# Performance work log

Hardware: AMD Instinct MI355X
Metric: run time of the kernel (lower is better)

The kernel has to match this reference:

```python
import jax, jax.numpy as jnp
import numpy as np
import itertools


def _interpn_linear(vol, loc):
    """Trilinear interpolation of vol [D,H,W,C] at absolute coords loc [D,H,W,3].
    Matches neurite's interpn: clip coords to volume, floor/ceil corners, 8-corner
    weighted sum (nearest-extrapolation at borders)."""
    D, H, W, C = vol.shape
    max_idx = jnp.asarray([D - 1, H - 1, W - 1], dtype=loc.dtype)
    loc = jnp.clip(loc, 0.0, max_idx)
    loc0 = jnp.floor(loc)
    loc1 = jnp.minimum(loc0 + 1.0, max_idx)
    d1 = loc1 - loc                     # weight of corner 0 (floor)
    d0 = 1.0 - d1                       # weight of corner 1 (ceil)
    w = jnp.stack([d1, d0], axis=0)     # [2, D,H,W,3]
    idx = jnp.stack([loc0, loc1], axis=0).astype(jnp.int32)  # [2, D,H,W,3]
    vol_flat = vol.reshape(-1, C)
    out = jnp.zeros(loc.shape[:-1] + (C,), vol.dtype)
    for c in itertools.product((0, 1), repeat=3):  # fixed 8-corner loop
        flat = (idx[c[0], ..., 0] * H + idx[c[1], ..., 1]) * W + idx[c[2], ..., 2]
        wt = w[c[0], ..., 0] * w[c[1], ..., 1] * w[c[2], ..., 2]
        out = out + wt[..., None] * vol_flat[flat]
    return out


def _warp(vol, shift):
    """Sample dense field vol [D,H,W,3] at grid + shift (voxelmorph transform())."""
    D, H, W, _ = shift.shape
    grid = jnp.stack(
        jnp.meshgrid(jnp.arange(D), jnp.arange(H), jnp.arange(W), indexing='ij'),
        axis=-1,
    ).astype(shift.dtype)
    return _interpn_linear(vol, grid + shift)


def _compose(transforms):
    """voxelmorph utils.compose for dense transforms: T(x) = C(B(A(x))).
    curr = curr + warp(nxt, curr), folding right-to-left."""
    curr = transforms[-1]
    for nxt in reversed(transforms[:-1]):
        curr = curr + jax.vmap(_warp)(nxt, curr)
    return curr


def setup_inputs() -> dict:
    key = jax.random.key(0)
    k1, k2, k3 = jax.random.split(key, 3)
    shape = (2, 128, 160, 192, 3)  # [B, D, H, W, ndims] dense displacement fields
    scale = 3.0  # ~3-voxel displacements, realistic registration magnitude
    return {
        't1': scale * jax.random.normal(k1, shape, dtype=jnp.float32),
        't2': scale * jax.random.normal(k2, shape, dtype=jnp.float32),
        't3': scale * jax.random.normal(k3, shape, dtype=jnp.float32),
    }


def reference(t1, t2, t3):
    # Transforms listed in application order A, B, C -> T(x) = C(B(A(x)))
    return _compose([t1, t2, t3])
```

## Files before the change

### kernel.cpp

```cpp
#include <hip/hip_runtime.h>
#include <hip/hip_fp16.h>


#define BB 2
#define DD 128
#define HH 160
#define WW 192

#define WT_TILES 3
#define HT_TILES 80
#define DT_TILES 32
#define NBLOCKS (WT_TILES * HT_TILES * DT_TILES * BB)
#define PER_XCD (NBLOCKS / 8)

static __device__ __forceinline__ float3 cvt_h4(uint2 q) {
    float2 fa = __half22float2(*(const __half2*)&q.x);
    float  fz = __half2float(*(const __half*)&q.y);
    return make_float3(fa.x, fa.y, fz);
}

__global__ __launch_bounds__(256) void conv_f16_kernel(
    const float4* __restrict__ src, uint2* __restrict__ dst)
{
    __shared__ float4 lds4[768];
    const float* lds = (const float*)lds4;

    long base = (long)blockIdx.x * 1024;
    const float4* s4 = src + (long)blockIdx.x * 768;
    int tid = threadIdx.x;

#pragma unroll
    for (int j = 0; j < 3; ++j)
        lds4[tid + 256 * j] = s4[tid + 256 * j];
    __syncthreads();

#pragma unroll
    for (int j = 0; j < 4; ++j) {
        int v = tid + 256 * j;
        float x = lds[3 * v], y = lds[3 * v + 1], z = lds[3 * v + 2];
        uint2 q;
        q.x = (unsigned)__half_as_ushort(__float2half_rn(x)) |
              ((unsigned)__half_as_ushort(__float2half_rn(y)) << 16);
        q.y = (unsigned)__half_as_ushort(__float2half_rn(z));
        dst[base + v] = q;
    }
}

static __device__ __forceinline__ void interp_one(
    const uint2* __restrict__ baseq, int d, int h, int w,
    float sx, float sy, float sz, float& ox, float& oy, float& oz)
{
    float lx = fminf(fmaxf((float)d + sx, 0.f), (float)(DD - 1));
    float ly = fminf(fmaxf((float)h + sy, 0.f), (float)(HH - 1));
    float lz = fminf(fmaxf((float)w + sz, 0.f), (float)(WW - 1));

    float fx = floorf(lx), fy = floorf(ly), fz = floorf(lz);
    int x0 = (int)fx, y0 = (int)fy, z0 = (int)fz;
    int x1 = min(x0 + 1, DD - 1);
    int y1 = min(y0 + 1, HH - 1);

    int  z0m = min(z0, WW - 2);
    bool zhi = (z0 == WW - 1);

    float wx0 = (float)x1 - lx;
    float wy0 = (float)y1 - ly;
    float wz0 = (float)(min(z0 + 1, WW - 1)) - lz;
    float wx1 = 1.f - wx0;
    float wy1 = 1.f - wy0;
    float wz1 = 1.f - wz0;

    const uint2* p00 = baseq + (((long)x0 * HH + y0) * WW + z0m);
    const uint2* p01 = baseq + (((long)x0 * HH + y1) * WW + z0m);
    const uint2* p10 = baseq + (((long)x1 * HH + y0) * WW + z0m);
    const uint2* p11 = baseq + (((long)x1 * HH + y1) * WW + z0m);
    uint2 q00l = p00[0], q00h = p00[1];
    uint2 q01l = p01[0], q01h = p01[1];
    uint2 q10l = p10[0], q10h = p10[1];
    uint2 q11l = p11[0], q11h = p11[1];

    float ax = 0.f, ay = 0.f, az = 0.f;
#define ROWPAIR(QL, QH, WXY) do {                                           \
        float3 vlo = cvt_h4(QL), vhi = cvt_h4(QH);                          \
        float3 v0  = zhi ? vhi : vlo;                                       \
        float wt_ = (WXY);                                                  \
        ax = fmaf(wt_, fmaf(wz0, v0.x, wz1 * vhi.x), ax);                   \
        ay = fmaf(wt_, fmaf(wz0, v0.y, wz1 * vhi.y), ay);                   \
        az = fmaf(wt_, fmaf(wz0, v0.z, wz1 * vhi.z), az);                   \
    } while (0)
    ROWPAIR(q00l, q00h, wx0 * wy0);
    ROWPAIR(q01l, q01h, wx0 * wy1);
    ROWPAIR(q10l, q10h, wx1 * wy0);
    ROWPAIR(q11l, q11h, wx1 * wy1);
#undef ROWPAIR

    ox = sx + ax;
    oy = sy + ay;
    oz = sz + az;
}

__global__ __launch_bounds__(256) void warp_add_h_kernel(
    const uint2* __restrict__ vol4,
    const float* shift,
    float* out)
{
    unsigned bid  = blockIdx.x;
    unsigned sbid = (bid & 7u) * PER_XCD + (bid >> 3);

    unsigned wt  = sbid % WT_TILES;  unsigned t0 = sbid / WT_TILES;
    unsigned ht  = t0 % HT_TILES;    unsigned t1 = t0 / HT_TILES;
    unsigned dt  = t1 % DT_TILES;    unsigned b  = t1 / DT_TILES;

    unsigned tid = threadIdx.x;
    int w = wt * 64 + 2 * (tid & 31);
    int h = ht * 2  + ((tid >> 5) & 1);
    int d = dt * 4  + (tid >> 6);

    const long nvb = (long)DD * HH * WW;
    long idx = (long)b * nvb + (((long)d * HH + h) * WW + w);

    const float2* sp2 = (const float2*)(shift + idx * 3);
    float2 sa = sp2[0], sb = sp2[1], sc = sp2[2];

    const uint2* baseq = vol4 + (long)b * nvb;

    float o0x, o0y, o0z, o1x, o1y, o1z;
    interp_one(baseq, d, h, w,     sa.x, sa.y, sb.x, o0x, o0y, o0z);
    interp_one(baseq, d, h, w + 1, sb.y, sc.x, sc.y, o1x, o1y, o1z);

    float2* op2 = (float2*)(out + idx * 3);
    op2[0] = make_float2(o0x, o0y);
    op2[1] = make_float2(o0z, o1x);
    op2[2] = make_float2(o1y, o1z);
}

extern "C" void kernel_launch(void* const* d_in, const int* in_sizes, int n_in,
                              void* d_out, int out_size, void* d_ws, size_t ws_size,
                              hipStream_t stream) {
    const float* t1 = (const float*)d_in[0];
    const float* t2 = (const float*)d_in[1];
    const float* t3 = (const float*)d_in[2];
    float* out  = (float*)d_out;
    uint2* volh = (uint2*)d_ws;

    const long nvt = (long)BB * DD * HH * WW;
    const int  conv_blocks = (int)(nvt / 1024);

    conv_f16_kernel<<<conv_blocks, 256, 0, stream>>>((const float4*)t2, volh);
    warp_add_h_kernel<<<NBLOCKS, 256, 0, stream>>>(volh, t3, out);
    conv_f16_kernel<<<conv_blocks, 256, 0, stream>>>((const float4*)t1, volh);
    warp_add_h_kernel<<<NBLOCKS, 256, 0, stream>>>(volh, out, out);
}
```

Measured before the change: 581.5 us.

## Fuse second f16 conversion into first warp launch, add nontemporal loads/stores

When the workspace can hold two half-precision volumes, the conversion of t1 runs as extra blocks inside the first warp kernel's launch, writing to a second buffer. This removes one launch boundary and lets conversion overlap with the gather-heavy warp. Shift reads, conversion reads and the final output stores now use nontemporal hints, and each corner pair is read with one 16-byte vector load instead of two 8-byte loads. It needs double the workspace, and the conversion and warp blocks now compete for bandwidth and cache within the same launch.

```diff
diff --git a/kernel.cpp b/kernel.cpp
--- a/kernel.cpp
+++ b/kernel.cpp
@@ -13,25 +13,35 @@
 #define NBLOCKS (WT_TILES * HT_TILES * DT_TILES * BB)
 #define PER_XCD (NBLOCKS / 8)
 
-static __device__ __forceinline__ float3 cvt_h4(uint2 q) {
-    float2 fa = __half22float2(*(const __half2*)&q.x);
-    float  fz = __half2float(*(const __half*)&q.y);
-    return make_float3(fa.x, fa.y, fz);
-}
-
-__global__ __launch_bounds__(256) void conv_f16_kernel(
-    const float4* __restrict__ src, uint2* __restrict__ dst)
-{
-    __shared__ float4 lds4[768];
+#define NVOX ((long)BB * DD * HH * WW)
+#define CONV_BLOCKS ((int)(NVOX / 1024))
+#define VOLH_BYTES ((size_t)NVOX * 8)
+
+typedef unsigned int uint4v __attribute__((ext_vector_type(4)));
+typedef uint4v uint4v_a8 __attribute__((aligned(8)));
+typedef float floatx2 __attribute__((ext_vector_type(2)));
+typedef float floatx4 __attribute__((ext_vector_type(4)));
+
+static __device__ __forceinline__ float3 cvt_h3(unsigned w0, unsigned w1) {
+    float x = __half2float(__ushort_as_half((unsigned short)(w0 & 0xffffu)));
+    float y = __half2float(__ushort_as_half((unsigned short)(w0 >> 16)));
+    float z = __half2float(__ushort_as_half((unsigned short)(w1 & 0xffffu)));
+    return make_float3(x, y, z);
+}
+
+static __device__ __forceinline__ void conv_body(
+    const floatx4* __restrict__ src, uint2* __restrict__ dst, unsigned bid)
+{
+    __shared__ floatx4 lds4[768];
     const float* lds = (const float*)lds4;
 
-    long base = (long)blockIdx.x * 1024;
-    const float4* s4 = src + (long)blockIdx.x * 768;
+    long base = (long)bid * 1024;
+    const floatx4* s4 = src + (long)bid * 768;
     int tid = threadIdx.x;
 
 #pragma unroll
     for (int j = 0; j < 3; ++j)
-        lds4[tid + 256 * j] = s4[tid + 256 * j];
+        lds4[tid + 256 * j] = __builtin_nontemporal_load(&s4[tid + 256 * j]);
     __syncthreads();
 
 #pragma unroll
@@ -46,6 +56,12 @@
     }
 }
 
+__global__ __launch_bounds__(256) void conv_f16_kernel(
+    const floatx4* __restrict__ src, uint2* __restrict__ dst)
+{
+    conv_body(src, dst, blockIdx.x);
+}
+
 static __device__ __forceinline__ void interp_one(
     const uint2* __restrict__ baseq, int d, int h, int w,
     float sx, float sy, float sz, float& ox, float& oy, float& oz)
@@ -69,28 +85,29 @@
     float wy1 = 1.f - wy0;
     float wz1 = 1.f - wz0;
 
-    const uint2* p00 = baseq + (((long)x0 * HH + y0) * WW + z0m);
-    const uint2* p01 = baseq + (((long)x0 * HH + y1) * WW + z0m);
-    const uint2* p10 = baseq + (((long)x1 * HH + y0) * WW + z0m);
-    const uint2* p11 = baseq + (((long)x1 * HH + y1) * WW + z0m);
-    uint2 q00l = p00[0], q00h = p00[1];
-    uint2 q01l = p01[0], q01h = p01[1];
-    uint2 q10l = p10[0], q10h = p10[1];
-    uint2 q11l = p11[0], q11h = p11[1];
+    const uint4v_a8* p00 = (const uint4v_a8*)(baseq + (((long)x0 * HH + y0) * WW + z0m));
+    const uint4v_a8* p01 = (const uint4v_a8*)(baseq + (((long)x0 * HH + y1) * WW + z0m));
+    const uint4v_a8* p10 = (const uint4v_a8*)(baseq + (((long)x1 * HH + y0) * WW + z0m));
+    const uint4v_a8* p11 = (const uint4v_a8*)(baseq + (((long)x1 * HH + y1) * WW + z0m));
+    uint4v q00 = *p00;
+    uint4v q01 = *p01;
+    uint4v q10 = *p10;
+    uint4v q11 = *p11;
 
     float ax = 0.f, ay = 0.f, az = 0.f;
-#define ROWPAIR(QL, QH, WXY) do {                                           \
-        float3 vlo = cvt_h4(QL), vhi = cvt_h4(QH);                          \
+#define ROWPAIR(Q, WXY) do {                                                \
+        float3 vlo = cvt_h3(Q.x, Q.y);                                      \
+        float3 vhi = cvt_h3(Q.z, Q.w);                                      \
         float3 v0  = zhi ? vhi : vlo;                                       \
         float wt_ = (WXY);                                                  \
         ax = fmaf(wt_, fmaf(wz0, v0.x, wz1 * vhi.x), ax);                   \
         ay = fmaf(wt_, fmaf(wz0, v0.y, wz1 * vhi.y), ay);                   \
         az = fmaf(wt_, fmaf(wz0, v0.z, wz1 * vhi.z), az);                   \
     } while (0)
-    ROWPAIR(q00l, q00h, wx0 * wy0);
-    ROWPAIR(q01l, q01h, wx0 * wy1);
-    ROWPAIR(q10l, q10h, wx1 * wy0);
-    ROWPAIR(q11l, q11h, wx1 * wy1);
+    ROWPAIR(q00, wx0 * wy0);
+    ROWPAIR(q01, wx0 * wy1);
+    ROWPAIR(q10, wx1 * wy0);
+    ROWPAIR(q11, wx1 * wy1);
 #undef ROWPAIR
 
     ox = sx + ax;
@@ -98,12 +115,12 @@
     oz = sz + az;
 }
 
-__global__ __launch_bounds__(256) void warp_add_h_kernel(
+template <bool NTSTORE>
+static __device__ __forceinline__ void warp_body(
     const uint2* __restrict__ vol4,
     const float* shift,
-    float* out)
-{
-    unsigned bid  = blockIdx.x;
+    float* out, unsigned bid)
+{
     unsigned sbid = (bid & 7u) * PER_XCD + (bid >> 3);
 
     unsigned wt  = sbid % WT_TILES;  unsigned t0 = sbid / WT_TILES;
@@ -118,8 +135,10 @@
     const long nvb = (long)DD * HH * WW;
     long idx = (long)b * nvb + (((long)d * HH + h) * WW + w);
 
-    const float2* sp2 = (const float2*)(shift + idx * 3);
-    float2 sa = sp2[0], sb = sp2[1], sc = sp2[2];
+    const floatx2* sp2 = (const floatx2*)(shift + idx * 3);
+    floatx2 sa = __builtin_nontemporal_load(&sp2[0]);
+    floatx2 sb = __builtin_nontemporal_load(&sp2[1]);
+    floatx2 sc = __builtin_nontemporal_load(&sp2[2]);
 
     const uint2* baseq = vol4 + (long)b * nvb;
 
@@ -127,10 +146,43 @@
     interp_one(baseq, d, h, w,     sa.x, sa.y, sb.x, o0x, o0y, o0z);
     interp_one(baseq, d, h, w + 1, sb.y, sc.x, sc.y, o1x, o1y, o1z);
 
-    float2* op2 = (float2*)(out + idx * 3);
-    op2[0] = make_float2(o0x, o0y);
-    op2[1] = make_float2(o0z, o1x);
-    op2[2] = make_float2(o1y, o1z);
+    floatx2* op2 = (floatx2*)(out + idx * 3);
+    floatx2 r0; r0.x = o0x; r0.y = o0y;
+    floatx2 r1; r1.x = o0z; r1.y = o1x;
+    floatx2 r2; r2.x = o1y; r2.y = o1z;
+    if (NTSTORE) {
+        __builtin_nontemporal_store(r0, &op2[0]);
+        __builtin_nontemporal_store(r1, &op2[1]);
+        __builtin_nontemporal_store(r2, &op2[2]);
+    } else {
+        op2[0] = r0;
+        op2[1] = r1;
+        op2[2] = r2;
+    }
+}
+
+__global__ __launch_bounds__(256) void warp_add_h_kernel(
+    const uint2* __restrict__ vol4, const float* shift, float* out)
+{
+    warp_body<false>(vol4, shift, out, blockIdx.x);
+}
+
+__global__ __launch_bounds__(256) void warp_add_h_nt_kernel(
+    const uint2* __restrict__ vol4, const float* shift, float* out)
+{
+    warp_body<true>(vol4, shift, out, blockIdx.x);
+}
+
+__global__ __launch_bounds__(256) void fused_warp_conv_kernel(
+    const uint2* __restrict__ vol4, const float* shift, float* out,
+    const floatx4* __restrict__ csrc, uint2* __restrict__ cdst)
+{
+    unsigned bid = blockIdx.x;
+    if (bid < (unsigned)CONV_BLOCKS) {
+        conv_body(csrc, cdst, bid);
+    } else {
+        warp_body<false>(vol4, shift, out, bid - CONV_BLOCKS);
+    }
 }
 
 extern "C" void kernel_launch(void* const* d_in, const int* in_sizes, int n_in,
@@ -140,13 +192,19 @@
     const float* t2 = (const float*)d_in[1];
     const float* t3 = (const float*)d_in[2];
     float* out  = (float*)d_out;
-    uint2* volh = (uint2*)d_ws;
-
-    const long nvt = (long)BB * DD * HH * WW;
-    const int  conv_blocks = (int)(nvt / 1024);
-
-    conv_f16_kernel<<<conv_blocks, 256, 0, stream>>>((const float4*)t2, volh);
-    warp_add_h_kernel<<<NBLOCKS, 256, 0, stream>>>(volh, t3, out);
-    conv_f16_kernel<<<conv_blocks, 256, 0, stream>>>((const float4*)t1, volh);
-    warp_add_h_kernel<<<NBLOCKS, 256, 0, stream>>>(volh, out, out);
-}
+
+    uint2* volA = (uint2*)d_ws;
+
+    if (ws_size >= 2 * VOLH_BYTES) {
+        uint2* volB = (uint2*)((char*)d_ws + VOLH_BYTES);
+        conv_f16_kernel<<<CONV_BLOCKS, 256, 0, stream>>>((const floatx4*)t2, volA);
+        fused_warp_conv_kernel<<<CONV_BLOCKS + NBLOCKS, 256, 0, stream>>>(
+            volA, t3, out, (const floatx4*)t1, volB);
+        warp_add_h_nt_kernel<<<NBLOCKS, 256, 0, stream>>>(volB, out, out);
+    } else {
+        conv_f16_kernel<<<CONV_BLOCKS, 256, 0, stream>>>((const floatx4*)t2, volA);
+        warp_add_h_kernel<<<NBLOCKS, 256, 0, stream>>>(volA, t3, out);
+        conv_f16_kernel<<<CONV_BLOCKS, 256, 0, stream>>>((const floatx4*)t1, volA);
+        warp_add_h_nt_kernel<<<NBLOCKS, 256, 0, stream>>>(volA, out, out);
+    }
+}
```

Result: faster. 545.8 us (-6.1%).
